# Kernel tuning notes

Measured on AMD Instinct MI355X. Metric: run time of the kernel, lower is better.

The kernel has to match this reference:

```python
import jax, jax.numpy as jnp
import numpy as np

B, T, E, HID, K = 64, 512, 768, 256, 11
H = HID // 2  # per-direction LSTM hidden = 128


def setup_inputs() -> dict:
    key = jax.random.key(0)
    ks = iter(jax.random.split(key, 40))

    def gn(shape, s=0.08):
        return jax.random.normal(next(ks), shape, jnp.float32) * s

    inp = {}
    inp["embeds"] = jax.random.normal(next(ks), (B, T, E), jnp.float32)
    inp["tags"] = jax.random.randint(next(ks), (B, T), 0, K)
    inp["mask"] = jnp.ones((B, T), jnp.bool_)
    # 2-layer bidirectional LSTM params, PyTorch layout: W_ih [4H, din], gate order i,f,g,o
    for l, din in ((0, E), (1, HID)):
        for sfx in ("", "_r"):
            inp[f"w_ih_l{l}{sfx}"] = gn((4 * H, din))
            inp[f"w_hh_l{l}{sfx}"] = gn((4 * H, H))
            inp[f"b_ih_l{l}{sfx}"] = gn((4 * H,))
            inp[f"b_hh_l{l}{sfx}"] = gn((4 * H,))
    inp["linear_w"] = gn((K, HID))
    inp["linear_b"] = gn((K,))
    inp["start_trans"] = gn((K,))
    inp["end_trans"] = gn((K,))
    inp["trans"] = gn((K, K))
    return inp


def _lstm_dir(xs, wih, whh, bih, bhh, reverse):
    # xs: [T, B, din] -> [T, B, H]; PyTorch gate order i, f, g, o
    Hn = whh.shape[1]
    h0 = jnp.zeros((xs.shape[1], Hn), xs.dtype)

    def step(carry, xt):
        h, c = carry
        g = xt @ wih.T + h @ whh.T + bih + bhh
        i, f, gg, o = jnp.split(g, 4, axis=-1)
        c = jax.nn.sigmoid(f) * c + jax.nn.sigmoid(i) * jnp.tanh(gg)
        h = jax.nn.sigmoid(o) * jnp.tanh(c)
        return (h, c), h

    _, hs = jax.lax.scan(step, (h0, h0), xs, reverse=reverse)
    return hs


def reference(embeds, tags, mask,
              w_ih_l0, w_hh_l0, b_ih_l0, b_hh_l0,
              w_ih_l0_r, w_hh_l0_r, b_ih_l0_r, b_hh_l0_r,
              w_ih_l1, w_hh_l1, b_ih_l1, b_hh_l1,
              w_ih_l1_r, w_hh_l1_r, b_ih_l1_r, b_hh_l1_r,
              linear_w, linear_b, start_trans, end_trans, trans):
    xs = jnp.transpose(embeds, (1, 0, 2))  # [T, B, E]
    # BiLSTM layer 0 and 1 (dropout p=0.1 is identity in eval/deterministic reference)
    h0 = jnp.concatenate([
        _lstm_dir(xs, w_ih_l0, w_hh_l0, b_ih_l0, b_hh_l0, False),
        _lstm_dir(xs, w_ih_l0_r, w_hh_l0_r, b_ih_l0_r, b_hh_l0_r, True)], axis=-1)
    h1 = jnp.concatenate([
        _lstm_dir(h0, w_ih_l1, w_hh_l1, b_ih_l1, b_hh_l1, False),
        _lstm_dir(h0, w_ih_l1_r, w_hh_l1_r, b_ih_l1_r, b_hh_l1_r, True)], axis=-1)
    em = h1 @ linear_w.T + linear_b  # emissions [T, B, K]

    tags_t = tags.T                    # [T, B]
    mask_f = mask.T.astype(em.dtype)   # [T, B]
    bidx = jnp.arange(em.shape[1])

    # ---- CRF numerator (gold path score), torchcrf semantics ----
    num = start_trans[tags_t[0]] + em[0, bidx, tags_t[0]]
    trans_sc = trans[tags_t[:-1], tags_t[1:]]                                   # [T-1, B]
    emit_sc = jnp.take_along_axis(em[1:], tags_t[1:, :, None], axis=2)[..., 0]  # [T-1, B]
    num = num + jnp.sum((trans_sc + emit_sc) * mask_f[1:], axis=0)
    seq_ends = jnp.sum(mask.astype(jnp.int32), axis=1) - 1
    num = num + end_trans[tags[bidx, seq_ends]]

    # ---- CRF denominator (log partition, forward algorithm as one scan) ----
    def fstep(score, xt):
        em_t, m_t = xt
        nxt = jax.nn.logsumexp(score[:, :, None] + trans[None] + em_t[:, None, :], axis=1)
        return jnp.where(m_t[:, None] > 0, nxt, score), None

    score, _ = jax.lax.scan(fstep, start_trans[None] + em[0], (em[1:], mask_f[1:]))
    den = jax.nn.logsumexp(score + end_trans[None], axis=1)

    # loss = -crf(emissions, tags, mask, reduction='mean')
    return -jnp.mean(num - den)
```

## Files before the change

### kernel.cpp

```cpp
#include <hip/hip_runtime.h>
#include <hip/hip_bf16.h>

typedef unsigned short u16;
typedef __bf16 bf16x8 __attribute__((ext_vector_type(8)));
typedef float f32x4 __attribute__((ext_vector_type(4)));
typedef u16 u16x8 __attribute__((ext_vector_type(8)));

__device__ __forceinline__ float bf2f(u16 u) {
    unsigned x = ((unsigned)u) << 16;
    return __builtin_bit_cast(float, x);
}
__device__ __forceinline__ u16 f2bf(float f) {
    unsigned x = __builtin_bit_cast(unsigned, f);
    unsigned r = (x + 0x7fffu + ((x >> 16) & 1u)) >> 16;
    return (u16)r;
}
__device__ __forceinline__ float sigm(float x) {
    return __builtin_amdgcn_rcpf(1.f + __expf(-x));
}
__device__ __forceinline__ float tanh_fast(float x) {
    return 1.f - 2.f * __builtin_amdgcn_rcpf(1.f + __expf(2.f * x));
}

__global__ void convw_kernel(const float* __restrict__ wf, const float* __restrict__ wr,
                             u16* __restrict__ out, int half_rows, int K) {
    int idx = blockIdx.x * 256 + threadIdx.x;
    int total = 2 * half_rows * K;
    if (idx >= total) return;
    int n = idx / K, k = idx - n * K;
    float v = (n < half_rows) ? wf[(size_t)n * K + k] : wr[(size_t)(n - half_rows) * K + k];
    out[idx] = f2bf(v);
}

template <bool AF32>
__global__ __launch_bounds__(256, 2) void gemm_bf16_bt(const void* __restrict__ Av,
                                                       const u16* __restrict__ B,
                                                       u16* __restrict__ C,
                                                       int M, int N, int K) {
    __shared__ __align__(16) u16 As[128 * 40];
    __shared__ __align__(16) u16 Bs[128 * 40];
    const int tid = threadIdx.x;
    const int n0 = blockIdx.x * 128, m0 = blockIdx.y * 128;
    const int srow = tid >> 1, shalf = tid & 1;
    const int lane = tid & 63, wv = tid >> 6;
    const int wm = wv >> 1, wn = wv & 1;
    const int frow = lane & 15, fko = (lane >> 4) * 8;
    f32x4 acc[4][4] = {};
    const int nk = K >> 5;
    for (int kt = 0; kt < nk; ++kt) {
        u16x8 a0, a1;
        if (AF32) {
            const float* ap = (const float*)Av + (size_t)(m0 + srow) * K + kt * 32 + shalf * 16;
            f32x4 f0 = *(const f32x4*)(ap);
            f32x4 f1 = *(const f32x4*)(ap + 4);
            f32x4 f2 = *(const f32x4*)(ap + 8);
            f32x4 f3 = *(const f32x4*)(ap + 12);
#pragma unroll
            for (int x = 0; x < 4; x++) {
                a0[x] = f2bf(f0[x]); a0[4 + x] = f2bf(f1[x]);
                a1[x] = f2bf(f2[x]); a1[4 + x] = f2bf(f3[x]);
            }
        } else {
            const u16* ap = (const u16*)Av + (size_t)(m0 + srow) * K + kt * 32 + shalf * 16;
            a0 = *(const u16x8*)(ap);
            a1 = *(const u16x8*)(ap + 8);
        }
        const u16* bp = B + (size_t)(n0 + srow) * K + kt * 32 + shalf * 16;
        u16x8 b0 = *(const u16x8*)(bp);
        u16x8 b1 = *(const u16x8*)(bp + 8);
        __syncthreads();
        *(u16x8*)&As[srow * 40 + shalf * 16] = a0;
        *(u16x8*)&As[srow * 40 + shalf * 16 + 8] = a1;
        *(u16x8*)&Bs[srow * 40 + shalf * 16] = b0;
        *(u16x8*)&Bs[srow * 40 + shalf * 16 + 8] = b1;
        __syncthreads();
        bf16x8 af[4], bfr[4];
#pragma unroll
        for (int mi = 0; mi < 4; mi++)
            af[mi] = *(const bf16x8*)&As[(wm * 64 + mi * 16 + frow) * 40 + fko];
#pragma unroll
        for (int ni = 0; ni < 4; ni++)
            bfr[ni] = *(const bf16x8*)&Bs[(wn * 64 + ni * 16 + frow) * 40 + fko];
#pragma unroll
        for (int mi = 0; mi < 4; mi++)
#pragma unroll
            for (int ni = 0; ni < 4; ni++)
                acc[mi][ni] = __builtin_amdgcn_mfma_f32_16x16x32_bf16(af[mi], bfr[ni], acc[mi][ni], 0, 0, 0);
    }
#pragma unroll
    for (int mi = 0; mi < 4; mi++)
#pragma unroll
        for (int ni = 0; ni < 4; ni++)
#pragma unroll
            for (int r = 0; r < 4; r++) {
                int row = m0 + wm * 64 + mi * 16 + (lane >> 4) * 4 + r;
                int col = n0 + wn * 64 + ni * 16 + (lane & 15);
                C[(size_t)row * N + col] = f2bf(acc[mi][ni][r]);
            }
}

__global__ __launch_bounds__(256, 1) void lstm_mfma(const u16* __restrict__ xproj,
                                                    const float* __restrict__ whh_f,
                                                    const float* __restrict__ whh_r,
                                                    const float* __restrict__ bih_f,
                                                    const float* __restrict__ bhh_f,
                                                    const float* __restrict__ bih_r,
                                                    const float* __restrict__ bhh_r,
                                                    u16* __restrict__ hout) {
    const int p = blockIdx.x;
    const int d = blockIdx.y;
    const int tid = threadIdx.x;
    const int w = tid >> 6, l = tid & 63;
    const float* whh = d ? whh_r : whh_f;
    const float* bih = d ? bih_r : bih_f;
    const float* bhh = d ? bhh_r : bhh_f;

    bf16x8 bf[8][4];
#pragma unroll
    for (int k = 0; k < 8; ++k) {
        const float* wr = whh + (size_t)((w + 4 * k) * 16 + (l & 15)) * 128;
#pragma unroll
        for (int c = 0; c < 4; ++c) {
            f32x4 x0 = *(const f32x4*)(wr + c * 32 + (l >> 4) * 8);
            f32x4 x1 = *(const f32x4*)(wr + c * 32 + (l >> 4) * 8 + 4);
            u16x8 t;
#pragma unroll
            for (int x = 0; x < 4; x++) { t[x] = f2bf(x0[x]); t[4 + x] = f2bf(x1[x]); }
            bf[k][c] = __builtin_bit_cast(bf16x8, t);
        }
    }

    const int jcol = l & 15, jg = (l >> 4) & 1, b = l >> 5;
    const int j = jg * 64 + w * 16 + jcol;
    float bias[4];
#pragma unroll
    for (int gt = 0; gt < 4; gt++) bias[gt] = bih[gt * 128 + j] + bhh[gt * 128 + j];

    __shared__ __align__(16) u16 h_lds[2][16 * 136];
    for (int i = tid; i < 2 * 16 * 136; i += 256) ((u16*)h_lds)[i] = 0;

    const u16* xb = xproj + (size_t)(2 * p + b) * 512 * 1024 + (size_t)d * 512 + j;
    u16 xv_e[4], xv_o[4];
    {
        const int t0 = d ? 511 : 0;
        const int t1 = d ? 510 : 1;
#pragma unroll
        for (int gt = 0; gt < 4; gt++) {
            xv_e[gt] = xb[(size_t)t0 * 1024 + gt * 128];
            xv_o[gt] = xb[(size_t)t1 * 1024 + gt * 128];
        }
    }
    float c_state = 0.f;
    u16* ho = hout + (size_t)(2 * p + b) * 512 * 256 + (size_t)d * 128 + j;
    __syncthreads();

#define LSTM_STEP(BUF_R, BUF_W, XV, S_CUR, S_PRE)                                              \
    {                                                                                          \
        const int tt = d ? (511 - (S_CUR)) : (S_CUR);                                          \
        bf16x8 af[4];                                                                          \
        _Pragma("unroll") for (int c = 0; c < 4; ++c)                                          \
            af[c] = *(const bf16x8*)&h_lds[BUF_R][(l & 15) * 136 + c * 32 + (l >> 4) * 8];     \
        f32x4 acc[8];                                                                          \
        _Pragma("unroll") for (int k = 0; k < 8; ++k)                                          \
            acc[k] = __builtin_amdgcn_mfma_f32_16x16x32_bf16(af[0], bf[k][0],                  \
                                                             (f32x4){0.f, 0.f, 0.f, 0.f}, 0, 0, 0); \
        _Pragma("unroll") for (int c = 1; c < 4; ++c)                                          \
            _Pragma("unroll") for (int k = 0; k < 8; ++k)                                      \
                acc[k] = __builtin_amdgcn_mfma_f32_16x16x32_bf16(af[c], bf[k][c], acc[k], 0, 0, 0); \
        float gval[4];                                                                         \
        _Pragma("unroll") for (int gt = 0; gt < 4; gt++) {                                     \
            float x00 = __shfl(acc[2 * gt][0], jcol, 64);                                      \
            float x10 = __shfl(acc[2 * gt + 1][0], jcol, 64);                                  \
            float x01 = __shfl(acc[2 * gt][1], jcol, 64);                                      \
            float x11 = __shfl(acc[2 * gt + 1][1], jcol, 64);                                  \
            float xa = jg ? x10 : x00;                                                         \
            float xc = jg ? x11 : x01;                                                         \
            gval[gt] = (b ? xc : xa) + bf2f(XV[gt]) + bias[gt];                                \
        }                                                                                      \
        {                                                                                      \
            const int sp = (S_PRE) & 511;                                                      \
            const int tp = d ? (511 - sp) : sp;                                                \
            _Pragma("unroll") for (int gt = 0; gt < 4; gt++)                                   \
                XV[gt] = xb[(size_t)tp * 1024 + gt * 128];                                     \
        }                                                                                      \
        float ip = sigm(gval[0]), fp = sigm(gval[1]);                                          \
        float tg = tanh_fast(gval[2]), op = sigm(gval[3]);                                     \
        c_state = fp * c_state + ip * tg;                                                      \
        float hh = op * tanh_fast(c_state);                                                    \
        u16 hb = f2bf(hh);                                                                     \
        h_lds[BUF_W][b * 136 + j] = hb;                                                        \
        ho[(size_t)tt * 256] = hb;                                                             \
        asm volatile("s_waitcnt lgkmcnt(0)" ::: "memory");                                     \
        __builtin_amdgcn_sched_barrier(0);                                                     \
        __builtin_amdgcn_s_barrier();                                                          \
        __builtin_amdgcn_sched_barrier(0);                                                     \
    }

    for (int s = 0; s < 512; s += 2) {
        LSTM_STEP(0, 1, xv_e, s, s + 2)
        LSTM_STEP(1, 0, xv_o, s + 1, s + 3)
    }
#undef LSTM_STEP
}

__global__ __launch_bounds__(256) void em_kernel(const u16* __restrict__ h1,
                                                 const float* __restrict__ lw,
                                                 const float* __restrict__ lb,
                                                 float* __restrict__ em) {
    __shared__ float w[11 * 256];
    for (int i = threadIdx.x; i < 11 * 256; i += 256) w[i] = lw[i];
    __syncthreads();
    int r = blockIdx.x * 256 + threadIdx.x;
    const u16x8* hp = (const u16x8*)(h1 + (size_t)r * 256);
    float acc[11];
#pragma unroll
    for (int j = 0; j < 11; j++) acc[j] = lb[j];
    for (int kc = 0; kc < 32; ++kc) {
        u16x8 hv = hp[kc];
        float hf[8];
#pragma unroll
        for (int x = 0; x < 8; x++) hf[x] = bf2f(hv[x]);
#pragma unroll
        for (int x = 0; x < 8; x++)
#pragma unroll
            for (int j = 0; j < 11; j++) acc[j] = fmaf(hf[x], w[j * 256 + kc * 8 + x], acc[j]);
    }
    int b = r >> 9, t = r & 511;
    float* o = em + ((size_t)t * 64 + b) * 16;
#pragma unroll
    for (int j = 0; j < 11; j++) o[j] = acc[j];
}

__global__ __launch_bounds__(64) void crf_kernel(const float* __restrict__ em,
                                                 const int* __restrict__ tags,
                                                 const float* __restrict__ start_trans,
                                                 const float* __restrict__ end_trans,
                                                 const float* __restrict__ trans,
                                                 float* __restrict__ pb) {
    const int lane = threadIdx.x;
    const int seg = lane >> 4, kp = lane & 15;
    const int kpc = kp < 11 ? kp : 10;
    const int b = blockIdx.x * 4 + seg;
    const int* tg = tags + (size_t)b * 512;
    float num = 0.f;
    for (int t = kp; t < 512; t += 16) {
        int cur = tg[t];
        float e = em[((size_t)t * 64 + b) * 16 + cur];
        float tr = (t == 0) ? start_trans[cur] : trans[tg[t - 1] * 11 + cur];
        num += e + tr;
    }
#pragma unroll
    for (int off = 8; off >= 1; off >>= 1) num += __shfl_down(num, off, 16);
    float trcol[11];
#pragma unroll
    for (int k = 0; k < 11; k++) trcol[k] = trans[k * 11 + kpc];
    float s = start_trans[kpc] + em[(size_t)b * 16 + kpc];
    float em_nxt = em[((size_t)1 * 64 + b) * 16 + kpc];
    for (int t = 1; t < 512; ++t) {
        float em_t = em_nxt;
        int tn = (t + 1 < 512) ? t + 1 : t;
        em_nxt = em[((size_t)tn * 64 + b) * 16 + kpc];
        float v[11], m = -1e30f;
#pragma unroll
        for (int k = 0; k < 11; k++) {
            v[k] = __shfl(s, k, 16) + trcol[k];
            m = fmaxf(m, v[k]);
        }
        float sum = 0.f;
#pragma unroll
        for (int k = 0; k < 11; k++) sum += __expf(v[k] - m);
        s = m + __logf(sum) + em_t;
    }
    float u = s + end_trans[kpc];
    float m2 = -1e30f, vv[11];
#pragma unroll
    for (int k = 0; k < 11; k++) {
        vv[k] = __shfl(u, k, 16);
        m2 = fmaxf(m2, vv[k]);
    }
    float s2 = 0.f;
#pragma unroll
    for (int k = 0; k < 11; k++) s2 += __expf(vv[k] - m2);
    float den = m2 + __logf(s2);
    if (kp == 0) {
        float numt = num + end_trans[tg[511]];
        pb[b] = numt - den;
    }
}

__global__ __launch_bounds__(64) void final_kernel(const float* __restrict__ pb, float* __restrict__ out) {
    float v = pb[threadIdx.x];
#pragma unroll
    for (int off = 32; off >= 1; off >>= 1) v += __shfl_down(v, off, 64);
    if (threadIdx.x == 0) out[0] = -(v / 64.f);
}

extern "C" void kernel_launch(void* const* d_in, const int* in_sizes, int n_in,
                              void* d_out, int out_size, void* d_ws, size_t ws_size,
                              hipStream_t stream) {
    const float* embeds = (const float*)d_in[0];
    const int* tags = (const int*)d_in[1];
    const float* wih0f = (const float*)d_in[3];
    const float* whh0f = (const float*)d_in[4];
    const float* bih0f = (const float*)d_in[5];
    const float* bhh0f = (const float*)d_in[6];
    const float* wih0r = (const float*)d_in[7];
    const float* whh0r = (const float*)d_in[8];
    const float* bih0r = (const float*)d_in[9];
    const float* bhh0r = (const float*)d_in[10];
    const float* wih1f = (const float*)d_in[11];
    const float* whh1f = (const float*)d_in[12];
    const float* bih1f = (const float*)d_in[13];
    const float* bhh1f = (const float*)d_in[14];
    const float* wih1r = (const float*)d_in[15];
    const float* whh1r = (const float*)d_in[16];
    const float* bih1r = (const float*)d_in[17];
    const float* bhh1r = (const float*)d_in[18];
    const float* lw = (const float*)d_in[19];
    const float* lb = (const float*)d_in[20];
    const float* st = (const float*)d_in[21];
    const float* et = (const float*)d_in[22];
    const float* tr = (const float*)d_in[23];
    float* out = (float*)d_out;

    char* ws = (char*)d_ws;
    u16* xproj = (u16*)(ws + 0);
    u16* h0 = (u16*)(ws + 67108864);
    u16* h1 = (u16*)(ws + 83886080);
    float* em = (float*)(ws + 100663296);
    u16* w0c = (u16*)(ws + 102760448);
    u16* w1c = (u16*)(ws + 104333312);
    float* pb = (float*)(ws + 104857600);

    convw_kernel<<<3072, 256, 0, stream>>>(wih0f, wih0r, w0c, 512, 768);
    convw_kernel<<<1024, 256, 0, stream>>>(wih1f, wih1r, w1c, 512, 256);
    gemm_bf16_bt<true><<<dim3(8, 256), 256, 0, stream>>>(embeds, w0c, xproj, 32768, 1024, 768);
    lstm_mfma<<<dim3(32, 2), 256, 0, stream>>>(xproj, whh0f, whh0r, bih0f, bhh0f, bih0r, bhh0r, h0);
    gemm_bf16_bt<false><<<dim3(8, 256), 256, 0, stream>>>(h0, w1c, xproj, 32768, 1024, 256);
    lstm_mfma<<<dim3(32, 2), 256, 0, stream>>>(xproj, whh1f, whh1r, bih1f, bhh1f, bih1r, bhh1r, h1);
    em_kernel<<<128, 256, 0, stream>>>(h1, lw, lb, em);
    crf_kernel<<<16, 64, 0, stream>>>(em, tags, st, et, tr, pb);
    final_kernel<<<1, 64, 0, stream>>>(pb, out);
}
```

Before: 1.244 ms.

## Pack eight sequences per LSTM block using full MFMA tile rows

```diff
diff --git a/kernel.cpp b/kernel.cpp
--- a/kernel.cpp
+++ b/kernel.cpp
@@ -107,7 +107,7 @@
                                                     const float* __restrict__ bih_r,
                                                     const float* __restrict__ bhh_r,
                                                     u16* __restrict__ hout) {
-    const int p = blockIdx.x;
+    const int q = blockIdx.x;
     const int d = blockIdx.y;
     const int tid = threadIdx.x;
     const int w = tid >> 6, l = tid & 63;
@@ -130,28 +130,37 @@
         }
     }
 
-    const int jcol = l & 15, jg = (l >> 4) & 1, b = l >> 5;
-    const int j = jg * 64 + w * 16 + jcol;
-    float bias[4];
-#pragma unroll
-    for (int gt = 0; gt < 4; gt++) bias[gt] = bih[gt * 128 + j] + bhh[gt * 128 + j];
+    const int col = l & 15, g = l >> 4;
+    float bias[2][4];
+#pragma unroll
+    for (int jg = 0; jg < 2; jg++)
+#pragma unroll
+        for (int gt = 0; gt < 4; gt++) {
+            int j = 64 * jg + 16 * w + col;
+            bias[jg][gt] = bih[gt * 128 + j] + bhh[gt * 128 + j];
+        }
 
     __shared__ __align__(16) u16 h_lds[2][16 * 136];
     for (int i = tid; i < 2 * 16 * 136; i += 256) ((u16*)h_lds)[i] = 0;
 
-    const u16* xb = xproj + (size_t)(2 * p + b) * 512 * 1024 + (size_t)d * 512 + j;
-    u16 xv_e[4], xv_o[4];
+    const u16* xb0 = xproj + ((size_t)(8 * q + 2 * g) * 512) * 1024 + (size_t)d * 512 + 16 * w + col;
+    u16 xv_e[16], xv_o[16];
     {
         const int t0 = d ? 511 : 0;
         const int t1 = d ? 510 : 1;
 #pragma unroll
-        for (int gt = 0; gt < 4; gt++) {
-            xv_e[gt] = xb[(size_t)t0 * 1024 + gt * 128];
-            xv_o[gt] = xb[(size_t)t1 * 1024 + gt * 128];
-        }
-    }
-    float c_state = 0.f;
-    u16* ho = hout + (size_t)(2 * p + b) * 512 * 256 + (size_t)d * 128 + j;
+        for (int r = 0; r < 2; r++)
+#pragma unroll
+            for (int jg = 0; jg < 2; jg++)
+#pragma unroll
+                for (int gt = 0; gt < 4; gt++) {
+                    size_t off = (size_t)r * 512 * 1024 + (size_t)gt * 128 + 64 * jg;
+                    xv_e[r * 8 + jg * 4 + gt] = xb0[(size_t)t0 * 1024 + off];
+                    xv_o[r * 8 + jg * 4 + gt] = xb0[(size_t)t1 * 1024 + off];
+                }
+    }
+    float cs[2][2] = {};
+    u16* ho0 = hout + ((size_t)(8 * q + 2 * g) * 512) * 256 + (size_t)d * 128 + 16 * w + col;
     __syncthreads();
 
 #define LSTM_STEP(BUF_R, BUF_W, XV, S_CUR, S_PRE)                                              \
@@ -167,29 +176,28 @@
         _Pragma("unroll") for (int c = 1; c < 4; ++c)                                          \
             _Pragma("unroll") for (int k = 0; k < 8; ++k)                                      \
                 acc[k] = __builtin_amdgcn_mfma_f32_16x16x32_bf16(af[c], bf[k][c], acc[k], 0, 0, 0); \
-        float gval[4];                                                                         \
-        _Pragma("unroll") for (int gt = 0; gt < 4; gt++) {                                     \
-            float x00 = __shfl(acc[2 * gt][0], jcol, 64);                                      \
-            float x10 = __shfl(acc[2 * gt + 1][0], jcol, 64);                                  \
-            float x01 = __shfl(acc[2 * gt][1], jcol, 64);                                      \
-            float x11 = __shfl(acc[2 * gt + 1][1], jcol, 64);                                  \
-            float xa = jg ? x10 : x00;                                                         \
-            float xc = jg ? x11 : x01;                                                         \
-            gval[gt] = (b ? xc : xa) + bf2f(XV[gt]) + bias[gt];                                \
-        }                                                                                      \
+        _Pragma("unroll") for (int r = 0; r < 2; r++)                                          \
+            _Pragma("unroll") for (int jg = 0; jg < 2; jg++) {                                 \
+                float gv0 = acc[0 + jg][r] + bf2f(XV[r * 8 + jg * 4 + 0]) + bias[jg][0];       \
+                float gv1 = acc[2 + jg][r] + bf2f(XV[r * 8 + jg * 4 + 1]) + bias[jg][1];       \
+                float gv2 = acc[4 + jg][r] + bf2f(XV[r * 8 + jg * 4 + 2]) + bias[jg][2];       \
+                float gv3 = acc[6 + jg][r] + bf2f(XV[r * 8 + jg * 4 + 3]) + bias[jg][3];       \
+                cs[r][jg] = sigm(gv1) * cs[r][jg] + sigm(gv0) * tanh_fast(gv2);                \
+                float hh = sigm(gv3) * tanh_fast(cs[r][jg]);                                   \
+                u16 hb = f2bf(hh);                                                             \
+                h_lds[BUF_W][(g * 4 + r) * 136 + 64 * jg + 16 * w + col] = hb;                 \
+                ho0[(size_t)r * 512 * 256 + (size_t)tt * 256 + 64 * jg] = hb;                  \
+            }                                                                                  \
         {                                                                                      \
             const int sp = (S_PRE) & 511;                                                      \
             const int tp = d ? (511 - sp) : sp;                                                \
-            _Pragma("unroll") for (int gt = 0; gt < 4; gt++)                                   \
-                XV[gt] = xb[(size_t)tp * 1024 + gt * 128];                                     \
+            _Pragma("unroll") for (int r = 0; r < 2; r++)                                      \
+                _Pragma("unroll") for (int jg = 0; jg < 2; jg++)                               \
+                    _Pragma("unroll") for (int gt = 0; gt < 4; gt++)                           \
+                        XV[r * 8 + jg * 4 + gt] =                                              \
+                            xb0[(size_t)tp * 1024 + (size_t)r * 512 * 1024 +                   \
+                                (size_t)gt * 128 + 64 * jg];                                   \
         }                                                                                      \
-        float ip = sigm(gval[0]), fp = sigm(gval[1]);                                          \
-        float tg = tanh_fast(gval[2]), op = sigm(gval[3]);                                     \
-        c_state = fp * c_state + ip * tg;                                                      \
-        float hh = op * tanh_fast(c_state);                                                    \
-        u16 hb = f2bf(hh);                                                                     \
-        h_lds[BUF_W][b * 136 + j] = hb;                                                        \
-        ho[(size_t)tt * 256] = hb;                                                             \
         asm volatile("s_waitcnt lgkmcnt(0)" ::: "memory");                                     \
         __builtin_amdgcn_sched_barrier(0);                                                     \
         __builtin_amdgcn_s_barrier();                                                          \
@@ -335,9 +343,9 @@
     convw_kernel<<<3072, 256, 0, stream>>>(wih0f, wih0r, w0c, 512, 768);
     convw_kernel<<<1024, 256, 0, stream>>>(wih1f, wih1r, w1c, 512, 256);
     gemm_bf16_bt<true><<<dim3(8, 256), 256, 0, stream>>>(embeds, w0c, xproj, 32768, 1024, 768);
-    lstm_mfma<<<dim3(32, 2), 256, 0, stream>>>(xproj, whh0f, whh0r, bih0f, bhh0f, bih0r, bhh0r, h0);
+    lstm_mfma<<<dim3(8, 2), 256, 0, stream>>>(xproj, whh0f, whh0r, bih0f, bhh0f, bih0r, bhh0r, h0);
     gemm_bf16_bt<false><<<dim3(8, 256), 256, 0, stream>>>(h0, w1c, xproj, 32768, 1024, 256);
-    lstm_mfma<<<dim3(32, 2), 256, 0, stream>>>(xproj, whh1f, whh1r, bih1f, bhh1f, bih1r, bhh1r, h1);
+    lstm_mfma<<<dim3(8, 2), 256, 0, stream>>>(xproj, whh1f, whh1r, bih1f, bhh1f, bih1r, bhh1r, h1);
     em_kernel<<<128, 256, 0, stream>>>(h1, lw, lb, em);
     crf_kernel<<<16, 64, 0, stream>>>(em, tags, st, et, tr, pb);
     final_kernel<<<1, 64, 0, stream>>>(pb, out);
```

Result: slower. 1.401 ms (+12.6%).
